# Performance work log

Hardware: AMD Instinct MI355X
Metric: run time of the kernel (lower is better)

The kernel has to match this reference:

```python
import jax, jax.numpy as jnp
import numpy as np

R = 256            # rois_per_image = cfg.TRAIN.BATCH_SIZE
FG_QUOTA = 64      # round(FG_FRACTION=0.25 * R)
FG_THRESH = 0.5
BG_HI = 0.5
BG_LO = 0.0
MEANS = jnp.array([0.0, 0.0, 0.0, 0.0], jnp.float32)
STDS = jnp.array([0.1, 0.1, 0.2, 0.2], jnp.float32)
INSIDE_W = jnp.array([1.0, 1.0, 1.0, 1.0], jnp.float32)


def _iou(boxes, gt):
    # boxes [B,M,4], gt [B,G,4] -> IoU [B,M,G]  (bbox_overlaps_batch2)
    x1 = jnp.maximum(boxes[:, :, None, 0], gt[:, None, :, 0])
    y1 = jnp.maximum(boxes[:, :, None, 1], gt[:, None, :, 1])
    x2 = jnp.minimum(boxes[:, :, None, 2], gt[:, None, :, 2])
    y2 = jnp.minimum(boxes[:, :, None, 3], gt[:, None, :, 3])
    iw = jnp.clip(x2 - x1 + 1.0, 0.0)
    ih = jnp.clip(y2 - y1 + 1.0, 0.0)
    inter = iw * ih
    area_b = (boxes[..., 2] - boxes[..., 0] + 1.0) * (boxes[..., 3] - boxes[..., 1] + 1.0)
    area_g = (gt[..., 2] - gt[..., 0] + 1.0) * (gt[..., 3] - gt[..., 1] + 1.0)
    return inter / (area_b[:, :, None] + area_g[:, None, :] - inter)


def _bbox_transform(ex, gt):
    # bbox_transform_batch2: ex,gt [B,R,4] -> targets [B,R,4]
    ew = ex[..., 2] - ex[..., 0] + 1.0
    eh = ex[..., 3] - ex[..., 1] + 1.0
    ecx = ex[..., 0] + 0.5 * ew
    ecy = ex[..., 1] + 0.5 * eh
    gw = gt[..., 2] - gt[..., 0] + 1.0
    gh = gt[..., 3] - gt[..., 1] + 1.0
    gcx = gt[..., 0] + 0.5 * gw
    gcy = gt[..., 1] + 0.5 * gh
    return jnp.stack([(gcx - ecx) / ew, (gcy - ecy) / eh,
                      jnp.log(gw / ew), jnp.log(gh / eh)], axis=-1)


def setup_inputs() -> dict:
    key = jax.random.key(0)
    B, N, G, IMG = 16, 12000, 128, 800.0
    ks = jax.random.split(key, 8)

    def boxes(k1, k2, n):
        xy = jax.random.uniform(k1, (B, n, 2)) * (IMG - 260.0)
        wh = 16.0 + jax.random.uniform(k2, (B, n, 2)) * 240.0
        return jnp.concatenate([xy, xy + wh], axis=-1)

    roi_xy = boxes(ks[0], ks[1], N)
    bidx = jnp.broadcast_to(jnp.arange(B, dtype=jnp.float32)[:, None, None], (B, N, 1))
    all_rois = jnp.concatenate([bidx, roi_xy], axis=-1)  # [B,N,5]

    gt_xy = boxes(ks[2], ks[3], G)
    gt_lab = jax.random.randint(ks[4], (B, G, 1), 1, 151).astype(jnp.float32)
    gt_boxes = jnp.concatenate([gt_xy, gt_lab], axis=-1)  # [B,G,5]
    return {"all_rois": all_rois, "gt_boxes": gt_boxes}


def reference(all_rois, gt_boxes):
    B, N, _ = all_rois.shape
    G = gt_boxes.shape[1]
    bidx = jnp.arange(B, dtype=all_rois.dtype)

    # append gt boxes as extra proposals (first col = image index)
    gt_append = jnp.concatenate(
        [jnp.broadcast_to(bidx[:, None, None], (B, G, 1)), gt_boxes[:, :, :4]], axis=2)
    rois_all = jnp.concatenate([all_rois, gt_append], axis=1)  # [B,M,5], M=N+G

    ov = _iou(rois_all[..., 1:5], gt_boxes[..., :4])  # [B,M,G]
    max_ov = ov.max(axis=2)
    gt_asgn = ov.argmax(axis=2)
    labels = jnp.take_along_axis(gt_boxes[..., 4], gt_asgn, axis=1)  # [B,M]

    fg_mask = max_ov >= FG_THRESH
    bg_mask = (max_ov < BG_HI) & (max_ov >= BG_LO)

    # deterministic random sampling via keyed top_k (replaces np.random.permutation)
    k1, k2 = jax.random.split(jax.random.key(42))
    r1 = jax.random.uniform(k1, max_ov.shape)
    r2 = jax.random.uniform(k2, max_ov.shape)
    _, fg_top = jax.lax.top_k(jnp.where(fg_mask, r1 + 2.0, r1), R)  # fg first, randomized
    _, bg_top = jax.lax.top_k(jnp.where(bg_mask, r2 + 2.0, r2), R)

    fg_num = fg_mask.sum(axis=1)
    bg_num = bg_mask.sum(axis=1)
    fg_count = jnp.minimum(fg_num, FG_QUOTA)[:, None]          # [B,1]
    bg_avail = jnp.clip(bg_num, 1, R)[:, None]
    pos = jnp.broadcast_to(jnp.arange(R)[None, :], (B, R))

    fg_pick = jnp.take_along_axis(fg_top, jnp.minimum(pos, jnp.maximum(fg_count - 1, 0)), axis=1)
    bg_pick = jnp.take_along_axis(bg_top, (pos - fg_count) % bg_avail, axis=1)
    keep = jnp.where(pos < fg_count, fg_pick, bg_pick)         # [B,R]

    lab = jnp.take_along_axis(labels, keep, axis=1)
    lab = jnp.where(pos < fg_count, lab, 0.0)                  # bg -> class 0

    rois = jnp.take_along_axis(rois_all, keep[..., None], axis=1)  # [B,R,5]
    rois = rois.at[..., 0].set(bidx[:, None])

    asgn = jnp.take_along_axis(gt_asgn, keep, axis=1)
    gt_sel = jnp.take_along_axis(gt_boxes[..., :4], asgn[..., None], axis=1)

    t = (_bbox_transform(rois[..., 1:5], gt_sel) - MEANS) / STDS
    fg4 = (lab > 0).astype(t.dtype)[..., None]
    bbox_targets = t * fg4
    inside_w = fg4 * INSIDE_W
    outside_w = (inside_w > 0).astype(t.dtype)
    return rois, lab, bbox_targets, inside_w, outside_w
```

## Files before the change

kernel.cpp:

```cpp
#include <hip/hip_runtime.h>
#include <cstdint>
#include <cstddef>


#define THREEFRY_PARTITIONABLE 1

constexpr int kB = 16;
constexpr int kN = 12000;
constexpr int kG = 128;
constexpr int kM = kN + kG;
constexpr int kM4 = kM / 4;
constexpr int kR = 256;
constexpr int kFgQuota = 64;
constexpr unsigned kSeedHi = 0u;
constexpr unsigned kSeedLo = 42u;

__device__ __forceinline__ int imin(int a, int b) { return a < b ? a : b; }
__device__ __forceinline__ int imax(int a, int b) { return a > b ? a : b; }

__device__ __forceinline__ unsigned rotl32(unsigned v, int d) {
  return (v << d) | (v >> (32 - d));
}

__device__ __forceinline__ void tf2x32(unsigned k0, unsigned k1,
                                       unsigned x0, unsigned x1,
                                       unsigned& o0, unsigned& o1) {
  const unsigned k2 = k0 ^ k1 ^ 0x1BD11BDAu;
  x0 += k0; x1 += k1;
#define TF_R(d) x0 += x1; x1 = rotl32(x1, d); x1 ^= x0;
  TF_R(13) TF_R(15) TF_R(26) TF_R(6)
  x0 += k1; x1 += k2 + 1u;
  TF_R(17) TF_R(29) TF_R(16) TF_R(24)
  x0 += k2; x1 += k0 + 2u;
  TF_R(13) TF_R(15) TF_R(26) TF_R(6)
  x0 += k0; x1 += k1 + 3u;
  TF_R(17) TF_R(29) TF_R(16) TF_R(24)
  x0 += k1; x1 += k2 + 4u;
  TF_R(13) TF_R(15) TF_R(26) TF_R(6)
  x0 += k2; x1 += k0 + 5u;
#undef TF_R
  o0 = x0; o1 = x1;
}

__device__ __forceinline__ void derive_key(int which, unsigned& ka, unsigned& kb) {
#if THREEFRY_PARTITIONABLE
  unsigned a0, a1, b0, b1;
  tf2x32(kSeedHi, kSeedLo, 0u, 0u, a0, a1);
  tf2x32(kSeedHi, kSeedLo, 0u, 1u, b0, b1);
  ka = which ? b0 : a0;
  kb = which ? b1 : a1;
#else
  unsigned a0, a1, b0, b1;
  tf2x32(kSeedHi, kSeedLo, 0u, 2u, a0, a1);
  tf2x32(kSeedHi, kSeedLo, 1u, 3u, b0, b1);
  ka = which ? a1 : a0;
  kb = which ? b1 : b0;
#endif
}

__device__ __forceinline__ float bits_to_uniform(unsigned bits) {
  return __uint_as_float((bits >> 9) | 0x3f800000u) - 1.0f;
}

__device__ __forceinline__ float jax_uniform(unsigned ka, unsigned kb, unsigned i) {
#if THREEFRY_PARTITIONABLE
  unsigned o0, o1;
  tf2x32(ka, kb, 0u, i, o0, o1);
  return bits_to_uniform(o0 ^ o1);
#else
  const unsigned H = (unsigned)(kB * kM) / 2u;
  unsigned o0, o1;
  if (i < H) { tf2x32(ka, kb, i, i + H, o0, o1); return bits_to_uniform(o0); }
  else       { tf2x32(ka, kb, i - H, i, o0, o1); return bits_to_uniform(o1); }
#endif
}

__device__ __forceinline__ unsigned mask_bin(unsigned v) {
  unsigned bn = (v - 0x40000000u) >> 11;
  return bn > 2047u ? 2047u : bn;
}

__global__ __launch_bounds__(256) void k_prep(const float* __restrict__ all_rois,
                                              const float* __restrict__ gt_boxes,
                                              unsigned* __restrict__ vb) {
  __shared__ float4 sg[kG];
  __shared__ float sga[kG];
  __shared__ int s_fgp[2][128];
  const int b = blockIdx.y;
  const int tid = threadIdx.x;
  if (tid < kG) {
    const float* gp = gt_boxes + ((size_t)b * kG + tid) * 5;
    const float x0 = gp[0], y0 = gp[1], x1 = gp[2], y1 = gp[3];
    sg[tid] = make_float4(x0, y0, x1, y1);
    sga[tid] = ((x1 - x0) + 1.0f) * ((y1 - y0) + 1.0f);
  }
  const int rl = tid & 127;
  const int h = tid >> 7;
  const int m = blockIdx.x * 128 + rl;
  const bool valid = (m < kM);
  __syncthreads();

  float bx0 = 0.f, by0 = 0.f, bx1 = 0.f, by1 = 0.f;
  if (valid) {
    if (m < kN) {
      const float* rp = all_rois + ((size_t)b * kN + m) * 5;
      bx0 = rp[1]; by0 = rp[2]; bx1 = rp[3]; by1 = rp[4];
    } else {
      const float4 g4 = sg[m - kN];
      bx0 = g4.x; by0 = g4.y; bx1 = g4.z; by1 = g4.w;
    }
  }
  const float areab = ((bx1 - bx0) + 1.0f) * ((by1 - by0) + 1.0f);

  int fgp = 0;
  const int g0 = h * 64;
#pragma unroll 8
  for (int gg = 0; gg < 64; ++gg) {
    const int g = g0 + gg;
    const float4 g4 = sg[g];
    const float xx0 = fmaxf(bx0, g4.x);
    const float yy0 = fmaxf(by0, g4.y);
    const float xx1 = fminf(bx1, g4.z);
    const float yy1 = fminf(by1, g4.w);
    const float iw = fmaxf((xx1 - xx0) + 1.0f, 0.0f);
    const float ih = fmaxf((yy1 - yy0) + 1.0f, 0.0f);
    const float inter = iw * ih;
    const float denom = (areab + sga[g]) - inter;
    fgp |= (__builtin_fmaf(-0.5f, denom, inter) >= (-0x1p-26f) * denom) ? 1 : 0;
  }
  s_fgp[h][rl] = fgp;
  __syncthreads();
  if (!valid) return;
  const int fg = s_fgp[0][rl] | s_fgp[1][rl];

  unsigned ka, kb;
  derive_key(h, ka, kb);
  const unsigned i = (unsigned)(b * kM + m);
  const float r = jax_uniform(ka, kb, i);
  const float v = (fg ^ h) ? (r + 2.0f) : r;
  vb[(size_t)(h * kB + b) * kM + m] = __float_as_uint(v);
}

__device__ __forceinline__ int block_reduce_sum_w(int v, int* s_red, int tid, int nw) {
#pragma unroll
  for (int off = 32; off > 0; off >>= 1) v += __shfl_down(v, off, 64);
  __syncthreads();
  if ((tid & 63) == 0) s_red[tid >> 6] = v;
  __syncthreads();
  int t = 0;
  for (int w = 0; w < nw; ++w) t += s_red[w];
  return t;
}

__global__ __launch_bounds__(1024) void k_select(const unsigned* __restrict__ vb,
                                                 int* __restrict__ topidx,
                                                 int* __restrict__ nin) {
  __shared__ int s_hist[2048];
  __shared__ unsigned long long s_cand[1024];
  __shared__ int s_scan[256];
  __shared__ int s_red[16];
  __shared__ unsigned long long s_wmax[16];
  __shared__ int s_tbin, s_cnt;

  const int which = blockIdx.x;
  const int b = blockIdx.y;
  const int tid = threadIdx.x;
  const unsigned* src = vb + (size_t)(which * kB + b) * kM;
  const uint4* src4 = (const uint4*)src;
  int* dst = topidx + (size_t)(which * kB + b) * kR;

  for (int i = tid; i < 2048; i += 1024) s_hist[i] = 0;
  if (tid == 0) s_cnt = 0;
  __syncthreads();

  for (int i = tid; i < kM4; i += 1024) {
    const uint4 u = src4[i];
#define HBIN(x) if ((x) >= 0x40000000u) atomicAdd(&s_hist[mask_bin(x)], 1);
    HBIN(u.x) HBIN(u.y) HBIN(u.z) HBIN(u.w)
#undef HBIN
  }
  __syncthreads();

  int s = 0;
  if (tid < 256) {
    const int base = 2048 - 8 * (tid + 1);
#pragma unroll
    for (int j = 0; j < 8; ++j) s += s_hist[base + j];
    s_scan[tid] = s;
  }
  const int n_in = block_reduce_sum_w((tid < 256) ? s : 0, s_red, tid, 16);
  if (tid == 0) nin[which * kB + b] = n_in;
  const int quota = (which == 0) ? kFgQuota : kR;
  const int K = imin(n_in, quota);

  if (K == 0) {
    if (which == 0) return;
    unsigned long long best = 0ull;
    for (int m = tid; m < kM; m += 1024) {
      const unsigned long long key =
          ((unsigned long long)src[m] << 32) | (unsigned)(0xFFFFFFFFu - (unsigned)m);
      if (key > best) best = key;
    }
#pragma unroll
    for (int off = 32; off > 0; off >>= 1) {
      const unsigned long long o = __shfl_down(best, off, 64);
      if (o > best) best = o;
    }
    __syncthreads();
    if ((tid & 63) == 0) s_wmax[tid >> 6] = best;
    __syncthreads();
    if (tid == 0) {
      for (int w = 1; w < 16; ++w) if (s_wmax[w] > best) best = s_wmax[w];
      dst[0] = (int)(0xFFFFFFFFu - (unsigned)(best & 0xFFFFFFFFull));
    }
    return;
  }

  __syncthreads();
  for (int off = 1; off < 256; off <<= 1) {
    int add = 0;
    if (tid < 256 && tid >= off) add = s_scan[tid - off];
    __syncthreads();
    if (tid < 256) s_scan[tid] += add;
    __syncthreads();
  }
  if (tid < 256) {
    const int base = 2048 - 8 * (tid + 1);
    int s2 = 0;
#pragma unroll
    for (int j = 0; j < 8; ++j) s2 += s_hist[base + j];
    const int above = s_scan[tid] - s2;
    int cum = above;
    for (int j = 7; j >= 0; --j) {
      const int c = s_hist[base + j];
      if (cum < K && cum + c >= K) s_tbin = base + j;
      cum += c;
    }
  }
  __syncthreads();
  const unsigned tbin = (unsigned)s_tbin;

  for (int i = tid; i < kM4; i += 1024) {
    const uint4 u = src4[i];
#define CAND(x, j)                                                         \
    if ((x) >= 0x40000000u && mask_bin(x) >= tbin) {                       \
      const int p = atomicAdd(&s_cnt, 1);                                  \
      if (p < 1024)                                                        \
        s_cand[p] = ((unsigned long long)(x) << 32) |                      \
                    (unsigned)(0xFFFFFFFFu - (unsigned)(4 * i + (j)));     \
    }
    CAND(u.x, 0) CAND(u.y, 1) CAND(u.z, 2) CAND(u.w, 3)
#undef CAND
  }
  __syncthreads();
  const int Nc = imin(s_cnt, 1024);

  for (int j = tid; j < Nc; j += 1024) {
    const unsigned long long key = s_cand[j];
    int rank = 0;
    for (int i = 0; i < Nc; ++i) rank += (s_cand[i] > key) ? 1 : 0;
    if (rank < K)
      dst[rank] = (int)(0xFFFFFFFFu - (unsigned)(key & 0xFFFFFFFFull));
  }
}

__global__ __launch_bounds__(256) void k_final(const float* __restrict__ all_rois,
                                               const float* __restrict__ gt_boxes,
                                               const int* __restrict__ topidx,
                                               const int* __restrict__ nin,
                                               float* __restrict__ out) {
  const int lane = threadIdx.x & 63;
  const int idx = (blockIdx.x << 2) | (threadIdx.x >> 6);
  const int b = idx >> 8;
  const int pos = idx & 255;

  const int fgc = imin(nin[b], kFgQuota);
  const int bgav = imin(imax(nin[kB + b], 1), kR);
  const bool isfg = pos < fgc;
  int keep;
  if (isfg) keep = topidx[(size_t)b * kR + imin(pos, imax(fgc - 1, 0))];
  else      keep = topidx[(size_t)(kB + b) * kR + (pos - fgc) % bgav];

  const float* bp = (keep < kN) ? (all_rois + ((size_t)b * kN + keep) * 5 + 1)
                                : (gt_boxes + ((size_t)b * kG + (keep - kN)) * 5);
  const float bx0 = bp[0], by0 = bp[1], bx1 = bp[2], by1 = bp[3];
  const float areab = ((bx1 - bx0) + 1.0f) * ((by1 - by0) + 1.0f);

  unsigned long long best = 0ull;
#pragma unroll
  for (int h = 0; h < 2; ++h) {
    const int g = lane + 64 * h;
    const float* gp = gt_boxes + ((size_t)b * kG + g) * 5;
    const float gx0 = gp[0], gy0 = gp[1], gx1 = gp[2], gy1 = gp[3];
    const float ga = ((gx1 - gx0) + 1.0f) * ((gy1 - gy0) + 1.0f);
    const float xx0 = fmaxf(bx0, gx0);
    const float yy0 = fmaxf(by0, gy0);
    const float xx1 = fminf(bx1, gx1);
    const float yy1 = fminf(by1, gy1);
    const float iw = fmaxf((xx1 - xx0) + 1.0f, 0.0f);
    const float ih = fmaxf((yy1 - yy0) + 1.0f, 0.0f);
    const float inter = iw * ih;
    const float iou = inter / ((areab + ga) - inter);
    const unsigned long long key =
        ((unsigned long long)__float_as_uint(iou) << 7) | (unsigned)(127 - g);
    if (key > best) best = key;
  }
#pragma unroll
  for (int off = 1; off < 64; off <<= 1) {
    const unsigned long long o = __shfl_xor(best, off, 64);
    if (o > best) best = o;
  }
  const int a = 127 - (int)(best & 127ull);

  const float* gp = gt_boxes + ((size_t)b * kG + a) * 5;
  const float gx0 = gp[0], gy0 = gp[1], gx1 = gp[2], gy1 = gp[3];
  const float lab = isfg ? gp[4] : 0.0f;
  const float fg4 = (lab > 0.0f) ? 1.0f : 0.0f;

  const float ew = (bx1 - bx0) + 1.0f;
  const float eh = (by1 - by0) + 1.0f;
  const float ecx = bx0 + 0.5f * ew;
  const float ecy = by0 + 0.5f * eh;
  const float gw = (gx1 - gx0) + 1.0f;
  const float gh = (gy1 - gy0) + 1.0f;
  const float gcx = gx0 + 0.5f * gw;
  const float gcy = gy0 + 0.5f * gh;
  const float t0 = ((gcx - ecx) / ew) / 0.1f;
  const float t1 = ((gcy - ecy) / eh) / 0.1f;
  const float t2 = logf(gw / ew) / 0.2f;
  const float t3 = logf(gh / eh) / 0.2f;

  if (lane == 0) {
    float* o_rois = out;
    float* o_lab  = out + (size_t)kB * kR * 5;
    float* o_tgt  = o_lab + (size_t)kB * kR;
    float* o_iw   = o_tgt + (size_t)kB * kR * 4;
    float* o_ow   = o_iw  + (size_t)kB * kR * 4;
    const size_t p = (size_t)b * kR + pos;
    o_rois[p * 5 + 0] = (float)b;
    o_rois[p * 5 + 1] = bx0;
    o_rois[p * 5 + 2] = by0;
    o_rois[p * 5 + 3] = bx1;
    o_rois[p * 5 + 4] = by1;
    o_lab[p] = lab;
    o_tgt[p * 4 + 0] = t0 * fg4;
    o_tgt[p * 4 + 1] = t1 * fg4;
    o_tgt[p * 4 + 2] = t2 * fg4;
    o_tgt[p * 4 + 3] = t3 * fg4;
    o_iw[p * 4 + 0] = fg4; o_iw[p * 4 + 1] = fg4;
    o_iw[p * 4 + 2] = fg4; o_iw[p * 4 + 3] = fg4;
    o_ow[p * 4 + 0] = fg4; o_ow[p * 4 + 1] = fg4;
    o_ow[p * 4 + 2] = fg4; o_ow[p * 4 + 3] = fg4;
  }
}

extern "C" void kernel_launch(void* const* d_in, const int* in_sizes, int n_in_args,
                              void* d_out, int out_size, void* d_ws, size_t ws_size,
                              hipStream_t stream) {
  (void)in_sizes; (void)n_in_args; (void)out_size; (void)ws_size;
  const float* all_rois = (const float*)d_in[0];
  const float* gt_boxes = (const float*)d_in[1];
  float* out = (float*)d_out;

  char* ws = (char*)d_ws;
  unsigned* vb = (unsigned*)ws;
  int* topidx  = (int*)(ws + 1572864);
  int* nin     = (int*)(ws + 1572864 + 32768);

  dim3 gA((kM + 127) / 128, kB);
  k_prep<<<gA, 256, 0, stream>>>(all_rois, gt_boxes, vb);
  dim3 gB(2, kB);
  k_select<<<gB, 1024, 0, stream>>>(vb, topidx, nin);
  k_final<<<1024, 256, 0, stream>>>(all_rois, gt_boxes, topidx, nin, out);
}
```

Before: 87.50 us.

## Fuse top-k selection and final target computation into one per-image kernel

Merges the selection kernel and the final output kernel into one block per image. That block handles both the fg and bg halves, keeps its scores in registers so the input is read once instead of twice, and stores the chosen indices and GT data in shared memory. The prep kernel also splits the GT loop four ways with 64 boxes per block, which doubles the block count for more parallelism. The fusion removes one launch and the global round trip for topidx/nin. The cost is that the final stage now runs on only 16 blocks instead of 1024, so it has far less parallelism.

```diff
diff --git a/kernel.cpp b/kernel.cpp
--- a/kernel.cpp
+++ b/kernel.cpp
@@ -85,7 +85,7 @@
                                               unsigned* __restrict__ vb) {
   __shared__ float4 sg[kG];
   __shared__ float sga[kG];
-  __shared__ int s_fgp[2][128];
+  __shared__ int s_fgp[4][64];
   const int b = blockIdx.y;
   const int tid = threadIdx.x;
   if (tid < kG) {
@@ -94,9 +94,9 @@
     sg[tid] = make_float4(x0, y0, x1, y1);
     sga[tid] = ((x1 - x0) + 1.0f) * ((y1 - y0) + 1.0f);
   }
-  const int rl = tid & 127;
-  const int h = tid >> 7;
-  const int m = blockIdx.x * 128 + rl;
+  const int rl = tid & 63;
+  const int h = tid >> 6;
+  const int m = blockIdx.x * 64 + rl;
   const bool valid = (m < kM);
   __syncthreads();
 
@@ -113,9 +113,9 @@
   const float areab = ((bx1 - bx0) + 1.0f) * ((by1 - by0) + 1.0f);
 
   int fgp = 0;
-  const int g0 = h * 64;
+  const int g0 = h * 32;
 #pragma unroll 8
-  for (int gg = 0; gg < 64; ++gg) {
+  for (int gg = 0; gg < 32; ++gg) {
     const int g = g0 + gg;
     const float4 g4 = sg[g];
     const float xx0 = fmaxf(bx0, g4.x);
@@ -130,8 +130,8 @@
   }
   s_fgp[h][rl] = fgp;
   __syncthreads();
-  if (!valid) return;
-  const int fg = s_fgp[0][rl] | s_fgp[1][rl];
+  if (!valid || h >= 2) return;
+  const int fg = s_fgp[0][rl] | s_fgp[1][rl] | s_fgp[2][rl] | s_fgp[3][rl];
 
   unsigned ka, kb;
   derive_key(h, ka, kb);
@@ -141,216 +141,239 @@
   vb[(size_t)(h * kB + b) * kM + m] = __float_as_uint(v);
 }
 
-__device__ __forceinline__ int block_reduce_sum_w(int v, int* s_red, int tid, int nw) {
-#pragma unroll
-  for (int off = 32; off > 0; off >>= 1) v += __shfl_down(v, off, 64);
-  __syncthreads();
-  if ((tid & 63) == 0) s_red[tid >> 6] = v;
-  __syncthreads();
-  int t = 0;
-  for (int w = 0; w < nw; ++w) t += s_red[w];
-  return t;
-}
-
-__global__ __launch_bounds__(1024) void k_select(const unsigned* __restrict__ vb,
-                                                 int* __restrict__ topidx,
-                                                 int* __restrict__ nin) {
-  __shared__ int s_hist[2048];
-  __shared__ unsigned long long s_cand[1024];
-  __shared__ int s_scan[256];
+__global__ __launch_bounds__(1024) void k_selfin(const float* __restrict__ all_rois,
+                                                 const float* __restrict__ gt_boxes,
+                                                 const unsigned* __restrict__ vb,
+                                                 float* __restrict__ out) {
+  __shared__ float4 sg[kG];
+  __shared__ float sga[kG];
+  __shared__ float slab[kG];
+  __shared__ int s_hist[2][2048];
+  __shared__ unsigned long long s_cand[2][1024];
+  __shared__ int s_top[2][kR];
+  __shared__ int s_scan[2][256];
   __shared__ int s_red[16];
   __shared__ unsigned long long s_wmax[16];
-  __shared__ int s_tbin, s_cnt;
-
-  const int which = blockIdx.x;
-  const int b = blockIdx.y;
+  __shared__ int s_nin[2], s_tbin[2], s_cnt[2];
+
+  const int b = blockIdx.x;
   const int tid = threadIdx.x;
-  const unsigned* src = vb + (size_t)(which * kB + b) * kM;
-  const uint4* src4 = (const uint4*)src;
-  int* dst = topidx + (size_t)(which * kB + b) * kR;
-
-  for (int i = tid; i < 2048; i += 1024) s_hist[i] = 0;
-  if (tid == 0) s_cnt = 0;
-  __syncthreads();
-
-  for (int i = tid; i < kM4; i += 1024) {
-    const uint4 u = src4[i];
-#define HBIN(x) if ((x) >= 0x40000000u) atomicAdd(&s_hist[mask_bin(x)], 1);
-    HBIN(u.x) HBIN(u.y) HBIN(u.z) HBIN(u.w)
+  const int w = tid >> 6;
+  const int lane = tid & 63;
+  const int c = tid >> 9;
+  const int lt = tid & 511;
+
+  if (tid < kG) {
+    const float* gp = gt_boxes + ((size_t)b * kG + tid) * 5;
+    const float x0 = gp[0], y0 = gp[1], x1 = gp[2], y1 = gp[3];
+    sg[tid] = make_float4(x0, y0, x1, y1);
+    sga[tid] = ((x1 - x0) + 1.0f) * ((y1 - y0) + 1.0f);
+    slab[tid] = gp[4];
+  }
+  for (int i = tid; i < 4096; i += 1024) ((int*)s_hist)[i] = 0;
+  if (tid < 2) s_cnt[tid] = 0;
+  __syncthreads();
+
+  const uint4* src4 = (const uint4*)(vb + (size_t)(c * kB + b) * kM);
+  uint4 cache[6];
+  int cnt = 0;
+#pragma unroll
+  for (int k = 0; k < 6; ++k) {
+    const int i = lt + (k << 9);
+    if (i < kM4) {
+      const uint4 u = src4[i];
+      cache[k] = u;
+#define HBIN(x) if ((x) >= 0x40000000u) { ++cnt; atomicAdd(&s_hist[c][mask_bin(x)], 1); }
+      HBIN(u.x) HBIN(u.y) HBIN(u.z) HBIN(u.w)
 #undef HBIN
-  }
-  __syncthreads();
+    } else {
+      cache[k] = make_uint4(0u, 0u, 0u, 0u);
+    }
+  }
+#pragma unroll
+  for (int off = 32; off > 0; off >>= 1) cnt += __shfl_down(cnt, off, 64);
+  if (lane == 0) s_red[w] = cnt;
+  __syncthreads();
+  if (lt == 0) {
+    int t = 0;
+    for (int ww = c * 8; ww < c * 8 + 8; ++ww) t += s_red[ww];
+    s_nin[c] = t;
+  }
+  __syncthreads();
+  const int quota = (c == 0) ? kFgQuota : kR;
+  const int K = imin(s_nin[c], quota);
 
   int s = 0;
-  if (tid < 256) {
-    const int base = 2048 - 8 * (tid + 1);
-#pragma unroll
-    for (int j = 0; j < 8; ++j) s += s_hist[base + j];
-    s_scan[tid] = s;
-  }
-  const int n_in = block_reduce_sum_w((tid < 256) ? s : 0, s_red, tid, 16);
-  if (tid == 0) nin[which * kB + b] = n_in;
-  const int quota = (which == 0) ? kFgQuota : kR;
-  const int K = imin(n_in, quota);
-
-  if (K == 0) {
-    if (which == 0) return;
+  if (lt < 256) {
+    const int base = 2048 - 8 * (lt + 1);
+#pragma unroll
+    for (int j = 0; j < 8; ++j) s += s_hist[c][base + j];
+    s_scan[c][lt] = s;
+  }
+  __syncthreads();
+  for (int off = 1; off < 256; off <<= 1) {
+    int add = 0;
+    if (lt < 256 && lt >= off) add = s_scan[c][lt - off];
+    __syncthreads();
+    if (lt < 256) s_scan[c][lt] += add;
+    __syncthreads();
+  }
+  if (lt < 256 && K > 0) {
+    const int base = 2048 - 8 * (lt + 1);
+    const int above = s_scan[c][lt] - s;
+    int cum = above;
+    for (int j = 7; j >= 0; --j) {
+      const int cc = s_hist[c][base + j];
+      if (cum < K && cum + cc >= K) s_tbin[c] = base + j;
+      cum += cc;
+    }
+  }
+  if (c == 1 && K == 0) {
     unsigned long long best = 0ull;
-    for (int m = tid; m < kM; m += 1024) {
-      const unsigned long long key =
-          ((unsigned long long)src[m] << 32) | (unsigned)(0xFFFFFFFFu - (unsigned)m);
-      if (key > best) best = key;
+#pragma unroll
+    for (int k = 0; k < 6; ++k) {
+      const int i = lt + (k << 9);
+      if (i < kM4) {
+        const unsigned xs[4] = {cache[k].x, cache[k].y, cache[k].z, cache[k].w};
+#pragma unroll
+        for (int j = 0; j < 4; ++j) {
+          const unsigned long long key = ((unsigned long long)xs[j] << 32) |
+              (unsigned)(0xFFFFFFFFu - (unsigned)(4 * i + j));
+          if (key > best) best = key;
+        }
+      }
     }
 #pragma unroll
     for (int off = 32; off > 0; off >>= 1) {
       const unsigned long long o = __shfl_down(best, off, 64);
       if (o > best) best = o;
     }
-    __syncthreads();
-    if ((tid & 63) == 0) s_wmax[tid >> 6] = best;
-    __syncthreads();
-    if (tid == 0) {
-      for (int w = 1; w < 16; ++w) if (s_wmax[w] > best) best = s_wmax[w];
-      dst[0] = (int)(0xFFFFFFFFu - (unsigned)(best & 0xFFFFFFFFull));
-    }
-    return;
-  }
-
-  __syncthreads();
-  for (int off = 1; off < 256; off <<= 1) {
-    int add = 0;
-    if (tid < 256 && tid >= off) add = s_scan[tid - off];
-    __syncthreads();
-    if (tid < 256) s_scan[tid] += add;
-    __syncthreads();
-  }
-  if (tid < 256) {
-    const int base = 2048 - 8 * (tid + 1);
-    int s2 = 0;
-#pragma unroll
-    for (int j = 0; j < 8; ++j) s2 += s_hist[base + j];
-    const int above = s_scan[tid] - s2;
-    int cum = above;
-    for (int j = 7; j >= 0; --j) {
-      const int c = s_hist[base + j];
-      if (cum < K && cum + c >= K) s_tbin = base + j;
-      cum += c;
-    }
-  }
-  __syncthreads();
-  const unsigned tbin = (unsigned)s_tbin;
-
-  for (int i = tid; i < kM4; i += 1024) {
-    const uint4 u = src4[i];
-#define CAND(x, j)                                                         \
-    if ((x) >= 0x40000000u && mask_bin(x) >= tbin) {                       \
-      const int p = atomicAdd(&s_cnt, 1);                                  \
-      if (p < 1024)                                                        \
-        s_cand[p] = ((unsigned long long)(x) << 32) |                      \
-                    (unsigned)(0xFFFFFFFFu - (unsigned)(4 * i + (j)));     \
-    }
-    CAND(u.x, 0) CAND(u.y, 1) CAND(u.z, 2) CAND(u.w, 3)
-#undef CAND
-  }
-  __syncthreads();
-  const int Nc = imin(s_cnt, 1024);
-
-  for (int j = tid; j < Nc; j += 1024) {
-    const unsigned long long key = s_cand[j];
-    int rank = 0;
-    for (int i = 0; i < Nc; ++i) rank += (s_cand[i] > key) ? 1 : 0;
-    if (rank < K)
-      dst[rank] = (int)(0xFFFFFFFFu - (unsigned)(key & 0xFFFFFFFFull));
-  }
-}
-
-__global__ __launch_bounds__(256) void k_final(const float* __restrict__ all_rois,
-                                               const float* __restrict__ gt_boxes,
-                                               const int* __restrict__ topidx,
-                                               const int* __restrict__ nin,
-                                               float* __restrict__ out) {
-  const int lane = threadIdx.x & 63;
-  const int idx = (blockIdx.x << 2) | (threadIdx.x >> 6);
-  const int b = idx >> 8;
-  const int pos = idx & 255;
-
-  const int fgc = imin(nin[b], kFgQuota);
-  const int bgav = imin(imax(nin[kB + b], 1), kR);
-  const bool isfg = pos < fgc;
-  int keep;
-  if (isfg) keep = topidx[(size_t)b * kR + imin(pos, imax(fgc - 1, 0))];
-  else      keep = topidx[(size_t)(kB + b) * kR + (pos - fgc) % bgav];
-
-  const float* bp = (keep < kN) ? (all_rois + ((size_t)b * kN + keep) * 5 + 1)
-                                : (gt_boxes + ((size_t)b * kG + (keep - kN)) * 5);
-  const float bx0 = bp[0], by0 = bp[1], bx1 = bp[2], by1 = bp[3];
-  const float areab = ((bx1 - bx0) + 1.0f) * ((by1 - by0) + 1.0f);
-
-  unsigned long long best = 0ull;
-#pragma unroll
-  for (int h = 0; h < 2; ++h) {
-    const int g = lane + 64 * h;
-    const float* gp = gt_boxes + ((size_t)b * kG + g) * 5;
-    const float gx0 = gp[0], gy0 = gp[1], gx1 = gp[2], gy1 = gp[3];
-    const float ga = ((gx1 - gx0) + 1.0f) * ((gy1 - gy0) + 1.0f);
-    const float xx0 = fmaxf(bx0, gx0);
-    const float yy0 = fmaxf(by0, gy0);
-    const float xx1 = fminf(bx1, gx1);
-    const float yy1 = fminf(by1, gy1);
-    const float iw = fmaxf((xx1 - xx0) + 1.0f, 0.0f);
-    const float ih = fmaxf((yy1 - yy0) + 1.0f, 0.0f);
-    const float inter = iw * ih;
-    const float iou = inter / ((areab + ga) - inter);
-    const unsigned long long key =
-        ((unsigned long long)__float_as_uint(iou) << 7) | (unsigned)(127 - g);
-    if (key > best) best = key;
-  }
-#pragma unroll
-  for (int off = 1; off < 64; off <<= 1) {
-    const unsigned long long o = __shfl_xor(best, off, 64);
-    if (o > best) best = o;
-  }
-  const int a = 127 - (int)(best & 127ull);
-
-  const float* gp = gt_boxes + ((size_t)b * kG + a) * 5;
-  const float gx0 = gp[0], gy0 = gp[1], gx1 = gp[2], gy1 = gp[3];
-  const float lab = isfg ? gp[4] : 0.0f;
-  const float fg4 = (lab > 0.0f) ? 1.0f : 0.0f;
-
-  const float ew = (bx1 - bx0) + 1.0f;
-  const float eh = (by1 - by0) + 1.0f;
-  const float ecx = bx0 + 0.5f * ew;
-  const float ecy = by0 + 0.5f * eh;
-  const float gw = (gx1 - gx0) + 1.0f;
-  const float gh = (gy1 - gy0) + 1.0f;
-  const float gcx = gx0 + 0.5f * gw;
-  const float gcy = gy0 + 0.5f * gh;
-  const float t0 = ((gcx - ecx) / ew) / 0.1f;
-  const float t1 = ((gcy - ecy) / eh) / 0.1f;
-  const float t2 = logf(gw / ew) / 0.2f;
-  const float t3 = logf(gh / eh) / 0.2f;
-
-  if (lane == 0) {
-    float* o_rois = out;
-    float* o_lab  = out + (size_t)kB * kR * 5;
-    float* o_tgt  = o_lab + (size_t)kB * kR;
-    float* o_iw   = o_tgt + (size_t)kB * kR * 4;
-    float* o_ow   = o_iw  + (size_t)kB * kR * 4;
-    const size_t p = (size_t)b * kR + pos;
-    o_rois[p * 5 + 0] = (float)b;
-    o_rois[p * 5 + 1] = bx0;
-    o_rois[p * 5 + 2] = by0;
-    o_rois[p * 5 + 3] = bx1;
-    o_rois[p * 5 + 4] = by1;
-    o_lab[p] = lab;
-    o_tgt[p * 4 + 0] = t0 * fg4;
-    o_tgt[p * 4 + 1] = t1 * fg4;
-    o_tgt[p * 4 + 2] = t2 * fg4;
-    o_tgt[p * 4 + 3] = t3 * fg4;
-    o_iw[p * 4 + 0] = fg4; o_iw[p * 4 + 1] = fg4;
-    o_iw[p * 4 + 2] = fg4; o_iw[p * 4 + 3] = fg4;
-    o_ow[p * 4 + 0] = fg4; o_ow[p * 4 + 1] = fg4;
-    o_ow[p * 4 + 2] = fg4; o_ow[p * 4 + 3] = fg4;
+    if (lane == 0) s_wmax[w] = best;
+  }
+  __syncthreads();
+  if (tid == 512 && K == 0) {
+    unsigned long long best = s_wmax[8];
+    for (int ww = 9; ww < 16; ++ww) if (s_wmax[ww] > best) best = s_wmax[ww];
+    s_top[1][0] = (int)(0xFFFFFFFFu - (unsigned)(best & 0xFFFFFFFFull));
+  }
+
+  if (K > 0) {
+    const unsigned tbin = (unsigned)s_tbin[c];
+#pragma unroll
+    for (int k = 0; k < 6; ++k) {
+      const int i = lt + (k << 9);
+      if (i < kM4) {
+        const unsigned xs[4] = {cache[k].x, cache[k].y, cache[k].z, cache[k].w};
+#pragma unroll
+        for (int j = 0; j < 4; ++j) {
+          const unsigned x = xs[j];
+          if (x >= 0x40000000u && mask_bin(x) >= tbin) {
+            const int p = atomicAdd(&s_cnt[c], 1);
+            if (p < 1024)
+              s_cand[c][p] = ((unsigned long long)x << 32) |
+                  (unsigned)(0xFFFFFFFFu - (unsigned)(4 * i + j));
+          }
+        }
+      }
+    }
+  }
+  __syncthreads();
+  if (K > 0) {
+    const int Nc = imin(s_cnt[c], 1024);
+    for (int j = lt; j < Nc; j += 512) {
+      const unsigned long long key = s_cand[c][j];
+      int rank = 0;
+      for (int i = 0; i < Nc; ++i) rank += (s_cand[c][i] > key) ? 1 : 0;
+      if (rank < K)
+        s_top[c][rank] = (int)(0xFFFFFFFFu - (unsigned)(key & 0xFFFFFFFFull));
+    }
+  }
+  __syncthreads();
+
+  const int fgc = imin(s_nin[0], kFgQuota);
+  const int bgav = imin(imax(s_nin[1], 1), kR);
+  float* o_rois = out;
+  float* o_lab  = out + (size_t)kB * kR * 5;
+  float* o_tgt  = o_lab + (size_t)kB * kR;
+  float* o_iw   = o_tgt + (size_t)kB * kR * 4;
+  float* o_ow   = o_iw  + (size_t)kB * kR * 4;
+
+  for (int q = 0; q < 16; ++q) {
+    const int pos = w * 16 + q;
+    const bool isfg = pos < fgc;
+    int keep;
+    if (isfg) keep = s_top[0][imin(pos, imax(fgc - 1, 0))];
+    else      keep = s_top[1][(pos - fgc) % bgav];
+
+    float bx0, by0, bx1, by1;
+    if (keep < kN) {
+      const float* rp = all_rois + ((size_t)b * kN + keep) * 5;
+      bx0 = rp[1]; by0 = rp[2]; bx1 = rp[3]; by1 = rp[4];
+    } else {
+      const float4 g4 = sg[keep - kN];
+      bx0 = g4.x; by0 = g4.y; bx1 = g4.z; by1 = g4.w;
+    }
+    const float areab = ((bx1 - bx0) + 1.0f) * ((by1 - by0) + 1.0f);
+
+    unsigned long long best = 0ull;
+#pragma unroll
+    for (int hh = 0; hh < 2; ++hh) {
+      const int g = lane + 64 * hh;
+      const float4 g4 = sg[g];
+      const float xx0 = fmaxf(bx0, g4.x);
+      const float yy0 = fmaxf(by0, g4.y);
+      const float xx1 = fminf(bx1, g4.z);
+      const float yy1 = fminf(by1, g4.w);
+      const float iw = fmaxf((xx1 - xx0) + 1.0f, 0.0f);
+      const float ih = fmaxf((yy1 - yy0) + 1.0f, 0.0f);
+      const float inter = iw * ih;
+      const float iou = inter / ((areab + sga[g]) - inter);
+      const unsigned long long key =
+          ((unsigned long long)__float_as_uint(iou) << 7) | (unsigned)(127 - g);
+      if (key > best) best = key;
+    }
+#pragma unroll
+    for (int off = 1; off < 64; off <<= 1) {
+      const unsigned long long o = __shfl_xor(best, off, 64);
+      if (o > best) best = o;
+    }
+    const int a = 127 - (int)(best & 127ull);
+
+    const float4 gt4 = sg[a];
+    const float gx0 = gt4.x, gy0 = gt4.y, gx1 = gt4.z, gy1 = gt4.w;
+    const float lab = isfg ? slab[a] : 0.0f;
+    const float fg4 = (lab > 0.0f) ? 1.0f : 0.0f;
+
+    const float ew = (bx1 - bx0) + 1.0f;
+    const float eh = (by1 - by0) + 1.0f;
+    const float ecx = bx0 + 0.5f * ew;
+    const float ecy = by0 + 0.5f * eh;
+    const float gw = (gx1 - gx0) + 1.0f;
+    const float gh = (gy1 - gy0) + 1.0f;
+    const float gcx = gx0 + 0.5f * gw;
+    const float gcy = gy0 + 0.5f * gh;
+    const float t0 = ((gcx - ecx) / ew) / 0.1f;
+    const float t1 = ((gcy - ecy) / eh) / 0.1f;
+    const float t2 = logf(gw / ew) / 0.2f;
+    const float t3 = logf(gh / eh) / 0.2f;
+
+    if (lane == 0) {
+      const size_t p = (size_t)b * kR + pos;
+      o_rois[p * 5 + 0] = (float)b;
+      o_rois[p * 5 + 1] = bx0;
+      o_rois[p * 5 + 2] = by0;
+      o_rois[p * 5 + 3] = bx1;
+      o_rois[p * 5 + 4] = by1;
+      o_lab[p] = lab;
+      o_tgt[p * 4 + 0] = t0 * fg4;
+      o_tgt[p * 4 + 1] = t1 * fg4;
+      o_tgt[p * 4 + 2] = t2 * fg4;
+      o_tgt[p * 4 + 3] = t3 * fg4;
+      o_iw[p * 4 + 0] = fg4; o_iw[p * 4 + 1] = fg4;
+      o_iw[p * 4 + 2] = fg4; o_iw[p * 4 + 3] = fg4;
+      o_ow[p * 4 + 0] = fg4; o_ow[p * 4 + 1] = fg4;
+      o_ow[p * 4 + 2] = fg4; o_ow[p * 4 + 3] = fg4;
+    }
   }
 }
 
@@ -362,14 +385,9 @@
   const float* gt_boxes = (const float*)d_in[1];
   float* out = (float*)d_out;
 
-  char* ws = (char*)d_ws;
-  unsigned* vb = (unsigned*)ws;
-  int* topidx  = (int*)(ws + 1572864);
-  int* nin     = (int*)(ws + 1572864 + 32768);
-
-  dim3 gA((kM + 127) / 128, kB);
+  unsigned* vb = (unsigned*)d_ws;
+
+  dim3 gA((kM + 63) / 64, kB);
   k_prep<<<gA, 256, 0, stream>>>(all_rois, gt_boxes, vb);
-  dim3 gB(2, kB);
-  k_select<<<gB, 1024, 0, stream>>>(vb, topidx, nin);
-  k_final<<<1024, 256, 0, stream>>>(all_rois, gt_boxes, topidx, nin, out);
-}
+  k_selfin<<<kB, 1024, 0, stream>>>(all_rois, gt_boxes, vb, out);
+}
```

Result: slower. 116.4 us (+33.1%).
